# Kernel tuning notes

Measured on AMD Instinct MI355X. Metric: run time of the kernel, lower is better.

## Reference

```python
import jax, jax.numpy as jnp
import numpy as np

DIM = 128
HEADS = 4
WIN = (2, 7, 7)
N = WIN[0] * WIN[1] * WIN[2]  # 98
NW = 64
B_ = 2048  # batch(32) * nW(64)
SCALE = (DIM // HEADS) ** -0.5


def _relative_position_index():
    d, h, w = WIN
    coords = np.stack(np.meshgrid(np.arange(d), np.arange(h), np.arange(w), indexing='ij'))
    cf = coords.reshape(3, -1)
    rel = (cf[:, :, None] - cf[:, None, :]).transpose(1, 2, 0)
    rel[:, :, 0] += d - 1
    rel[:, :, 1] += h - 1
    rel[:, :, 2] += w - 1
    rel[:, :, 0] *= (2 * h - 1) * (2 * w - 1)
    rel[:, :, 1] *= 2 * w - 1
    return rel.sum(-1).astype(np.int32)  # [N, N]


def setup_inputs() -> dict:
    key = jax.random.key(0)
    ks = jax.random.split(key, 8)
    table_rows = (2 * WIN[0] - 1) * (2 * WIN[1] - 1) * (2 * WIN[2] - 1)  # 507
    return {
        "x": jax.random.normal(ks[0], (B_, N, DIM), jnp.float32),
        "mask": jax.random.normal(ks[1], (NW, N, N), jnp.float32),
        "qkv_w": jax.random.normal(ks[2], (DIM, 3 * DIM), jnp.float32) * 0.02,
        "qkv_b": jnp.zeros((3 * DIM,), jnp.float32),
        "rel_bias_table": jax.random.normal(ks[3], (table_rows, HEADS), jnp.float32) * 0.02,
        "rel_index": jnp.asarray(_relative_position_index()),
        "proj_w": jax.random.normal(ks[4], (DIM, DIM), jnp.float32) * 0.02,
        "proj_b": jnp.zeros((DIM,), jnp.float32),
    }


def reference(x, mask, qkv_w, qkv_b, rel_bias_table, rel_index, proj_w, proj_b):
    B, n, C = x.shape
    H = HEADS
    hd = C // H
    qkv = x @ qkv_w + qkv_b                              # [B, N, 3C]
    qkv = qkv.reshape(B, n, 3, H, hd).transpose(2, 0, 3, 1, 4)  # [3, B, H, N, hd]
    q, k, v = qkv[0] * SCALE, qkv[1], qkv[2]
    attn = jnp.einsum('bhnd,bhmd->bhnm', q, k)           # [B, H, N, N]
    bias = rel_bias_table[rel_index.reshape(-1)].reshape(n, n, H).transpose(2, 0, 1)
    attn = attn + bias[None]
    nW = mask.shape[0]
    attn = attn.reshape(B // nW, nW, H, n, n) + mask[None, :, None]
    attn = attn.reshape(B, H, n, n)
    attn = jax.nn.softmax(attn, axis=-1)
    out = jnp.einsum('bhnm,bhmd->bnhd', attn, v).reshape(B, n, C)
    return out @ proj_w + proj_b
```

## Files before the change

kernel.cpp:

```cpp
#include <hip/hip_runtime.h>
#include <hip/hip_bf16.h>

typedef __bf16 bf16;
typedef __attribute__((ext_vector_type(8))) __bf16 bf16x8;
typedef __attribute__((ext_vector_type(4))) __bf16 bf16x4;
typedef __attribute__((ext_vector_type(2))) __bf16 bf16x2;
typedef __attribute__((ext_vector_type(4))) float f32x4;

#define NTOK 98
#define NP   112
#define DIM  128
#define NH   4
#define HD   32
#define SCALE_Q 0.17677669529663687f

#define SXP 136
#define SKP 40
#define SVP 136
#define SPP 136
#define SQP 40
#define STGP 40
#define HREG 2560

#define WS_WTQ  0ULL
#define WS_PT   98304ULL
#define WS_BM   131072ULL
#define WS_NEED 12976128ULL

__global__ __launch_bounds__(256) void prep3_kernel(
    const float* __restrict__ qkv_w, const float* __restrict__ proj_w,
    const float* __restrict__ table, const int* __restrict__ rel,
    const float* __restrict__ mask,
    bf16* __restrict__ WTq, bf16* __restrict__ PT2, float* __restrict__ bmt)
{
  int i = blockIdx.x * 256 + threadIdx.x;
  if (i < 384*128) {
    int n = i >> 7, k = i & 127;
    WTq[i] = (bf16)qkv_w[k*384 + n];
  } else if (i < 384*128 + 128*128) {
    int j = i - 384*128; int n = j >> 7, kp = j & 127;
    int blk = kp >> 5, jl = kp & 31;
    int dl = (jl >> 1) + 16*(jl & 1);
    PT2[j] = (bf16)proj_w[(blk*32 + dl)*128 + n];
  } else {
    int g = i - (384*128 + 128*128);
    if (g >= 64*4*112*112) return;
    int k = g % 112;
    int rest = g / 112;
    int q = rest % 112;
    int rest2 = rest / 112;
    int h = rest2 & 3;
    int w = rest2 >> 2;
    float v;
    if (k >= NTOK) v = -1.0e30f;
    else if (q >= NTOK) v = 0.f;
    else v = table[rel[q*98 + k]*4 + h] + mask[w*9604 + q*98 + k];
    bmt[g] = v;
  }
}

__global__ __launch_bounds__(256, 3) void fused_kernel(
    const float* __restrict__ x, const float* __restrict__ qkv_b,
    const float* __restrict__ proj_b,
    const bf16* __restrict__ WTq, const bf16* __restrict__ PT2,
    const float* __restrict__ bmt, float* __restrict__ out)
{
  __shared__ alignas(16) bf16 sA[NP*SXP];
  __shared__ alignas(16) bf16 sB[4*HREG];

  const int b = blockIdx.x, w = b & 63;
  const int tid = threadIdx.x;
  const int wave = tid >> 6, lane = tid & 63;
  const int quad = lane >> 4, l16 = lane & 15;
  const int h = wave;
  const f32x4 fzero = {0.f, 0.f, 0.f, 0.f};

  {
    const float* xb = x + (size_t)b * (NTOK*DIM);
    for (int i = tid; i < NTOK*32; i += 256) {
      int row = i >> 5, c4 = (i & 31) << 2;
      const float4 v = *(const float4*)(xb + row*DIM + c4);
      bf16x4 pk; pk[0]=(bf16)v.x; pk[1]=(bf16)v.y; pk[2]=(bf16)v.z; pk[3]=(bf16)v.w;
      *(bf16x4*)&sA[row*SXP + c4] = pk;
    }
    for (int i = tid; i < 14*32; i += 256) {
      int row = NTOK + (i >> 5), c4 = (i & 31) << 2;
      uint2 z; z.x = 0; z.y = 0;
      *(uint2*)&sA[row*SXP + c4] = z;
    }
  }
  __syncthreads();

  bf16* stg = sB + h*HREG;
  bf16x8 bk[7], aq[7], bv[2][4];

  {
    const int baseK = DIM + h*HD, baseQ = h*HD;
    bf16x8 wK0[4], wK1[4], wQ0[4], wQ1[4];
#pragma unroll
    for (int ks = 0; ks < 4; ++ks) {
      wK0[ks] = *(const bf16x8*)(WTq + (baseK + l16)*DIM + ks*32 + quad*8);
      wK1[ks] = *(const bf16x8*)(WTq + (baseK + 16 + l16)*DIM + ks*32 + quad*8);
      wQ0[ks] = *(const bf16x8*)(WTq + (baseQ + l16)*DIM + ks*32 + quad*8);
      wQ1[ks] = *(const bf16x8*)(WTq + (baseQ + 16 + l16)*DIM + ks*32 + quad*8);
    }
    const float cK0 = qkv_b[baseK + l16], cK1 = qkv_b[baseK + 16 + l16];
    const float cQ0 = qkv_b[baseQ + l16], cQ1 = qkv_b[baseQ + 16 + l16];
#pragma unroll
    for (int mt = 0; mt < 7; ++mt) {
      f32x4 k0 = fzero, k1 = fzero, q0 = fzero, q1 = fzero;
#pragma unroll
      for (int ks = 0; ks < 4; ++ks) {
        const bf16x8 a = *(const bf16x8*)&sA[(mt*16 + l16)*SXP + ks*32 + quad*8];
        k0 = __builtin_amdgcn_mfma_f32_16x16x32_bf16(a, wK0[ks], k0, 0, 0, 0);
        k1 = __builtin_amdgcn_mfma_f32_16x16x32_bf16(a, wK1[ks], k1, 0, 0, 0);
        q0 = __builtin_amdgcn_mfma_f32_16x16x32_bf16(a, wQ0[ks], q0, 0, 0, 0);
        q1 = __builtin_amdgcn_mfma_f32_16x16x32_bf16(a, wQ1[ks], q1, 0, 0, 0);
      }
#pragma unroll
      for (int r = 0; r < 4; ++r) {
        bf16x2 pk; pk[0] = (bf16)(k0[r] + cK0); pk[1] = (bf16)(k1[r] + cK1);
        *(bf16x2*)&stg[(quad*4 + r)*STGP + l16*2] = pk;
        bf16x2 pq; pq[0] = (bf16)((q0[r] + cQ0) * SCALE_Q);
        pq[1] = (bf16)((q1[r] + cQ1) * SCALE_Q);
        *(bf16x2*)&stg[(16 + quad*4 + r)*STGP + l16*2] = pq;
      }
      bk[mt] = *(const bf16x8*)&stg[l16*STGP + quad*8];
      aq[mt] = *(const bf16x8*)&stg[(16 + l16)*STGP + quad*8];
    }
  }

  {
    const int baseV = 2*DIM + h*HD;
    bf16x8 wV0[4], wV1[4];
#pragma unroll
    for (int ks = 0; ks < 4; ++ks) {
      wV0[ks] = *(const bf16x8*)(WTq + (baseV + l16)*DIM + ks*32 + quad*8);
      wV1[ks] = *(const bf16x8*)(WTq + (baseV + 16 + l16)*DIM + ks*32 + quad*8);
    }
    const float cV0 = qkv_b[baseV + l16], cV1 = qkv_b[baseV + 16 + l16];
#pragma unroll
    for (int ck = 0; ck < 4; ++ck) {
      bf16* vb = stg + (ck & 1)*1280;
#pragma unroll
      for (int hf = 0; hf < 2; ++hf) {
        const int mt = ck*2 + hf;
        if (mt < 7) {
          f32x4 a0 = fzero, a1 = fzero;
#pragma unroll
          for (int ks = 0; ks < 4; ++ks) {
            const bf16x8 a = *(const bf16x8*)&sA[(mt*16 + l16)*SXP + ks*32 + quad*8];
            a0 = __builtin_amdgcn_mfma_f32_16x16x32_bf16(a, wV0[ks], a0, 0, 0, 0);
            a1 = __builtin_amdgcn_mfma_f32_16x16x32_bf16(a, wV1[ks], a1, 0, 0, 0);
          }
          bf16x4 p0, p1;
#pragma unroll
          for (int r = 0; r < 4; ++r) { p0[r] = (bf16)(a0[r] + cV0); p1[r] = (bf16)(a1[r] + cV1); }
          *(bf16x4*)&vb[l16*STGP + hf*16 + quad*4] = p0;
          *(bf16x4*)&vb[(16 + l16)*STGP + hf*16 + quad*4] = p1;
        } else {
          uint2 z; z.x = 0; z.y = 0;
          *(uint2*)&vb[l16*STGP + hf*16 + quad*4] = z;
          *(uint2*)&vb[(16 + l16)*STGP + hf*16 + quad*4] = z;
        }
      }
      bv[0][ck] = *(const bf16x8*)&vb[l16*STGP + quad*8];
      bv[1][ck] = *(const bf16x8*)&vb[(16 + l16)*STGP + quad*8];
    }
  }
  __syncthreads();

  bf16* sP = stg;
  {
    int row = lane >> 2, c0 = 112 + ((lane & 3) << 2);
    uint2 z; z.x = 0; z.y = 0;
    *(uint2*)&sP[row*SPP + c0] = z;
  }
  const float* bmh = bmt + ((size_t)(w*4 + h))*(NP*NP);

#pragma unroll
  for (int mt = 0; mt < 7; ++mt) {
    f32x4 s[7];
#pragma unroll
    for (int nt = 0; nt < 7; ++nt)
      s[nt] = __builtin_amdgcn_mfma_f32_16x16x32_bf16(bk[nt], aq[mt], fzero, 0, 0, 0);
    const float* bq = bmh + (mt*16 + l16)*NP;
#pragma unroll
    for (int nt = 0; nt < 7; ++nt) {
      const f32x4 bm4 = *(const f32x4*)(bq + nt*16 + quad*4);
      s[nt] = s[nt] + bm4;
    }
#pragma unroll
    for (int nt = 0; nt < 7; ++nt)
#pragma unroll
      for (int r = 0; r < 4; ++r)
        s[nt][r] = __expf(s[nt][r]);
#pragma unroll
    for (int nt = 0; nt < 7; ++nt) {
      bf16x4 pk;
#pragma unroll
      for (int r = 0; r < 4; ++r) pk[r] = (bf16)s[nt][r];
      *(bf16x4*)&sP[l16*SPP + nt*16 + quad*4] = pk;
    }
    float rs[7];
#pragma unroll
    for (int nt = 0; nt < 7; ++nt)
      rs[nt] = (s[nt][0] + s[nt][1]) + (s[nt][2] + s[nt][3]);
    float sum = ((rs[0] + rs[1]) + (rs[2] + rs[3])) + ((rs[4] + rs[5]) + rs[6]);
    sum += __shfl_xor(sum, 16);
    sum += __shfl_xor(sum, 32);
    const float inv = __builtin_amdgcn_rcpf(sum);
    float invr[4];
#pragma unroll
    for (int r = 0; r < 4; ++r)
      invr[r] = __shfl(inv, quad*4 + r, 64);
    f32x4 o0 = fzero, o1 = fzero;
#pragma unroll
    for (int ks = 0; ks < 4; ++ks) {
      const bf16x8 ap = *(const bf16x8*)&sP[l16*SPP + ks*32 + quad*8];
      o0 = __builtin_amdgcn_mfma_f32_16x16x32_bf16(ap, bv[0][ks], o0, 0, 0, 0);
      o1 = __builtin_amdgcn_mfma_f32_16x16x32_bf16(ap, bv[1][ks], o1, 0, 0, 0);
    }
#pragma unroll
    for (int r = 0; r < 4; ++r) {
      bf16x2 ow; ow[0] = (bf16)(o0[r]*invr[r]); ow[1] = (bf16)(o1[r]*invr[r]);
      *(bf16x2*)&sA[(mt*16 + quad*4 + r)*SXP + h*HD + l16*2] = ow;
    }
  }
  __syncthreads();

  float* outb = out + (size_t)b * (NTOK*DIM);
#pragma unroll
  for (int nn = 0; nn < 2; ++nn) {
    const int nt2 = wave + nn*4;
    bf16x8 pf[4];
#pragma unroll
    for (int ks = 0; ks < 4; ++ks)
      pf[ks] = *(const bf16x8*)(PT2 + (nt2*16 + l16)*DIM + ks*32 + quad*8);
    const float pb = proj_b[nt2*16 + l16];
#pragma unroll
    for (int mt = 0; mt < 7; ++mt) {
      f32x4 acc = fzero;
#pragma unroll
      for (int ks = 0; ks < 4; ++ks) {
        const bf16x8 a = *(const bf16x8*)&sA[(mt*16 + l16)*SXP + ks*32 + quad*8];
        acc = __builtin_amdgcn_mfma_f32_16x16x32_bf16(a, pf[ks], acc, 0, 0, 0);
      }
#pragma unroll
      for (int r = 0; r < 4; ++r) {
        const int row = mt*16 + quad*4 + r;
        if (row < NTOK)
          outb[row*DIM + nt2*16 + l16] = acc[r] + pb;
      }
    }
  }
}


__global__ __launch_bounds__(256) void prep_kernel(
    const float* __restrict__ qkv_w, const float* __restrict__ proj_w,
    const float* __restrict__ table, const int* __restrict__ rel_index,
    bf16* __restrict__ WTq, bf16* __restrict__ PT, float* __restrict__ biasf)
{
  int i = blockIdx.x * 256 + threadIdx.x;
  if (i < 384*128) {
    int n = i >> 7, k = i & 127;
    WTq[i] = (bf16)qkv_w[k*384 + n];
  } else if (i < 384*128 + 128*128) {
    int j = i - 384*128; int n = j >> 7, k = j & 127;
    PT[j] = (bf16)proj_w[k*128 + n];
  } else if (i < 384*128 + 128*128 + 98*98) {
    int j = i - (384*128 + 128*128);
    int idx = rel_index[j];
#pragma unroll
    for (int h = 0; h < 4; ++h) biasf[h*9604 + j] = table[idx*4 + h];
  }
}

__global__ __launch_bounds__(512, 2) void win_attn_kernel(
    const float* __restrict__ x, const float* __restrict__ mask,
    const float* __restrict__ qkv_b, const float* __restrict__ proj_b,
    const bf16* __restrict__ WTq, const bf16* __restrict__ PT,
    const float* __restrict__ biasf, float* __restrict__ out)
{
  __shared__ bf16 sX[NP*SXP];
  __shared__ bf16 sK[NH*NP*SKP];
  __shared__ bf16 sVT[NH*HD*SVP];
  __shared__ bf16 sQs[8*16*SQP];
  __shared__ bf16 sPs[8*16*SPP];

  const int b = blockIdx.x;
  const int w = b & 63;
  const int tid = threadIdx.x;
  const int wave = tid >> 6, lane = tid & 63;
  const int quad = lane >> 4, l16 = lane & 15;
  const f32x4 fzero = {0.f, 0.f, 0.f, 0.f};

  {
    const float* xb = x + (size_t)b * (NTOK*DIM);
    for (int i = tid; i < NTOK*32; i += 512) {
      int row = i >> 5, c4 = (i & 31) << 2;
      const float4 v = *(const float4*)(xb + row*DIM + c4);
      bf16x4 pk; pk[0]=(bf16)v.x; pk[1]=(bf16)v.y; pk[2]=(bf16)v.z; pk[3]=(bf16)v.w;
      *(bf16x4*)&sX[row*SXP + c4] = pk;
    }
    for (int i = tid; i < 14*32; i += 512) {
      int row = NTOK + (i >> 5), c4 = (i & 31) << 2;
      uint2 z; z.x = 0; z.y = 0;
      *(uint2*)&sX[row*SXP + c4] = z;
    }
    {
      int h = tid >> 7, rem = tid & 127, d = rem >> 2, c0 = 112 + ((rem & 3) << 2);
      uint2 z; z.x = 0; z.y = 0;
      *(uint2*)&sVT[(h*HD + d)*SVP + c0] = z;
    }
  }
  __syncthreads();

#pragma unroll
  for (int j = 0; j < 2; ++j) {
    const int job = wave*2 + j;
    const int h = job >> 2, part = job & 3;
    const bool isK = part < 2;
    const int ncol = (isK ? DIM + h*HD + part*16 : 2*DIM + h*HD + (part-2)*16) + l16;
    bf16x8 bfr[4];
#pragma unroll
    for (int ks = 0; ks < 4; ++ks)
      bfr[ks] = *(const bf16x8*)(WTq + ncol*DIM + ks*32 + quad*8);
    const float cb = qkv_b[ncol];
#pragma unroll
    for (int mt = 0; mt < 7; ++mt) {
      f32x4 acc = fzero;
#pragma unroll
      for (int ks = 0; ks < 4; ++ks) {
        const bf16x8 a = *(const bf16x8*)&sX[(mt*16 + l16)*SXP + ks*32 + quad*8];
        acc = __builtin_amdgcn_mfma_f32_16x16x32_bf16(a, bfr[ks], acc, 0, 0, 0);
      }
      const int tb = mt*16 + quad*4;
      if (isK) {
        const int d = part*16 + l16;
#pragma unroll
        for (int r = 0; r < 4; ++r)
          sK[(h*NP + tb + r)*SKP + d] = (bf16)(acc[r] + cb);
      } else {
        const int d = (part-2)*16 + l16;
        bf16x4 pk;
#pragma unroll
        for (int r = 0; r < 4; ++r) pk[r] = (bf16)(acc[r] + cb);
        *(bf16x4*)&sVT[(h*HD + d)*SVP + tb] = pk;
      }
    }
  }
  __syncthreads();

  {
    const int h = wave >> 1, sub = wave & 1;
    bf16x8 qb[2][4];
#pragma unroll
    for (int nt2 = 0; nt2 < 2; ++nt2)
#pragma unroll
      for (int ks = 0; ks < 4; ++ks)
        qb[nt2][ks] = *(const bf16x8*)(WTq + (h*HD + nt2*16 + l16)*DIM + ks*32 + quad*8);
    const float qbias0 = qkv_b[h*HD + l16];
    const float qbias1 = qkv_b[h*HD + 16 + l16];
    bf16* sQ = sQs + wave*16*SQP;
    bf16* sP = sPs + wave*16*SPP;
    {
      int row = lane >> 2, c0 = 112 + ((lane & 3) << 2);
      uint2 z; z.x = 0; z.y = 0;
      *(uint2*)&sP[row*SPP + c0] = z;
    }
    const float* bias_h = biasf + h*9604;
    const float* mask_w = mask + w*9604;

    f32x4 oacc0 = fzero, oacc1 = fzero;
#pragma unroll 1
    for (int it = 0; it < 4; ++it) {
      const int mt = sub + it*2;
      const bool valid = mt < 7;
      if (valid) {
        f32x4 qa0 = fzero, qa1 = fzero;
#pragma unroll
        for (int ks = 0; ks < 4; ++ks) {
          const bf16x8 a = *(const bf16x8*)&sX[(mt*16 + l16)*SXP + ks*32 + quad*8];
          qa0 = __builtin_amdgcn_mfma_f32_16x16x32_bf16(a, qb[0][ks], qa0, 0, 0, 0);
          qa1 = __builtin_amdgcn_mfma_f32_16x16x32_bf16(a, qb[1][ks], qa1, 0, 0, 0);
        }
#pragma unroll
        for (int r = 0; r < 4; ++r) {
          sQ[(quad*4 + r)*SQP + l16]      = (bf16)((qa0[r] + qbias0) * SCALE_Q);
          sQ[(quad*4 + r)*SQP + 16 + l16] = (bf16)((qa1[r] + qbias1) * SCALE_Q);
        }
        const bf16x8 aq = *(const bf16x8*)&sQ[l16*SQP + quad*8];
        f32x4 s[7];
#pragma unroll
        for (int nt = 0; nt < 7; ++nt) {
          const bf16x8 bk2 = *(const bf16x8*)&sK[(h*NP + nt*16 + l16)*SKP + quad*8];
          s[nt] = __builtin_amdgcn_mfma_f32_16x16x32_bf16(aq, bk2, fzero, 0, 0, 0);
        }
#pragma unroll
        for (int r = 0; r < 4; ++r) {
          const int row = mt*16 + quad*4 + r;
          const bool rowok = row < NTOK;
          float mx = -3.0e38f;
#pragma unroll
          for (int nt = 0; nt < 7; ++nt) {
            const int col = nt*16 + l16;
            float sv;
            if (rowok && col < NTOK)
              sv = s[nt][r] + bias_h[row*NTOK + col] + mask_w[row*NTOK + col];
            else
              sv = -1.0e30f;
            s[nt][r] = sv;
            mx = fmaxf(mx, sv);
          }
#pragma unroll
          for (int off = 1; off < 16; off <<= 1)
            mx = fmaxf(mx, __shfl_xor(mx, off, 64));
          float sum = 0.f;
#pragma unroll
          for (int nt = 0; nt < 7; ++nt) {
            const float p = __expf(s[nt][r] - mx);
            s[nt][r] = p;
            sum += p;
          }
#pragma unroll
          for (int off = 1; off < 16; off <<= 1)
            sum += __shfl_xor(sum, off, 64);
          const float inv = __builtin_amdgcn_rcpf(sum);
#pragma unroll
          for (int nt = 0; nt < 7; ++nt)
            sP[(quad*4 + r)*SPP + nt*16 + l16] = (bf16)(s[nt][r] * inv);
        }
        oacc0 = fzero; oacc1 = fzero;
#pragma unroll
        for (int ks = 0; ks < 4; ++ks) {
          const bf16x8 ap = *(const bf16x8*)&sP[l16*SPP + ks*32 + quad*8];
          const bf16x8 bv0 = *(const bf16x8*)&sVT[(h*HD + l16)*SVP + ks*32 + quad*8];
          const bf16x8 bv1 = *(const bf16x8*)&sVT[(h*HD + 16 + l16)*SVP + ks*32 + quad*8];
          oacc0 = __builtin_amdgcn_mfma_f32_16x16x32_bf16(ap, bv0, oacc0, 0, 0, 0);
          oacc1 = __builtin_amdgcn_mfma_f32_16x16x32_bf16(ap, bv1, oacc1, 0, 0, 0);
        }
      }
      __syncthreads();
      if (valid) {
#pragma unroll
        for (int r = 0; r < 4; ++r) {
          sX[(mt*16 + quad*4 + r)*SXP + h*HD + l16]      = (bf16)(oacc0[r]);
          sX[(mt*16 + quad*4 + r)*SXP + h*HD + 16 + l16] = (bf16)(oacc1[r]);
        }
      }
    }
  }
  __syncthreads();

  {
    const int nt = wave;
    bf16x8 pbf[4];
#pragma unroll
    for (int ks = 0; ks < 4; ++ks)
      pbf[ks] = *(const bf16x8*)(PT + (nt*16 + l16)*DIM + ks*32 + quad*8);
    const float pb = proj_b[nt*16 + l16];
    float* outb = out + (size_t)b * (NTOK*DIM);
#pragma unroll
    for (int mt = 0; mt < 7; ++mt) {
      f32x4 acc = fzero;
#pragma unroll
      for (int ks = 0; ks < 4; ++ks) {
        const bf16x8 a = *(const bf16x8*)&sX[(mt*16 + l16)*SXP + ks*32 + quad*8];
        acc = __builtin_amdgcn_mfma_f32_16x16x32_bf16(a, pbf[ks], acc, 0, 0, 0);
      }
#pragma unroll
      for (int r = 0; r < 4; ++r) {
        const int row = mt*16 + quad*4 + r;
        if (row < NTOK)
          outb[row*DIM + nt*16 + l16] = acc[r] + pb;
      }
    }
  }
}

extern "C" void kernel_launch(void* const* d_in, const int* in_sizes, int n_in,
                              void* d_out, int out_size, void* d_ws, size_t ws_size,
                              hipStream_t stream)
{
  const float* x      = (const float*)d_in[0];
  const float* mask   = (const float*)d_in[1];
  const float* qkv_w  = (const float*)d_in[2];
  const float* qkv_b  = (const float*)d_in[3];
  const float* table  = (const float*)d_in[4];
  const int*   rel    = (const int*)d_in[5];
  const float* proj_w = (const float*)d_in[6];
  const float* proj_b = (const float*)d_in[7];
  float* out = (float*)d_out;
  char* ws = (char*)d_ws;

  if (ws_size >= WS_NEED) {
    bf16*  WTq = (bf16*)(ws + WS_WTQ);
    bf16*  PT2 = (bf16*)(ws + WS_PT);
    float* bmt = (float*)(ws + WS_BM);

    const int prep_total = 384*128 + 128*128 + 64*4*112*112;
    prep3_kernel<<<(prep_total + 255)/256, 256, 0, stream>>>(
        qkv_w, proj_w, table, rel, mask, WTq, PT2, bmt);
    fused_kernel<<<2048, 256, 0, stream>>>(x, qkv_b, proj_b, WTq, PT2, bmt, out);
  } else {
    bf16*  WTq   = (bf16*)(ws + WS_WTQ);
    bf16*  PT    = (bf16*)(ws + WS_PT);
    float* biasf = (float*)(ws + WS_BM);
    const int prep_total = 384*128 + 128*128 + 98*98;
    prep_kernel<<<(prep_total + 255)/256, 256, 0, stream>>>(qkv_w, proj_w, table, rel, WTq, PT, biasf);
    win_attn_kernel<<<2048, 512, 0, stream>>>(x, mask, qkv_b, proj_b, WTq, PT, biasf, out);
  }
}
```

Baseline: 281.3 us.

## Prefetch bias rows, use exp2 with folded log2e, add MFMA priority hints

The precomputed bias/mask table is now scaled by log2(e), and the Q scale absorbs log2(e), so the softmax can use the native exp2 instruction instead of __expf. The prep kernel writes the bias table four floats per thread with vector stores. In the attention loop, the next row-tile's bias is prefetched into registers while the current tile is processed, and the PV MFMA is issued before the row-sum reduction. s_setprio brackets around MFMA blocks favour matrix issue across waves. The cost is more live registers, which could hurt occupancy at 3 blocks per SM.

```diff
diff --git a/kernel.cpp b/kernel.cpp
--- a/kernel.cpp
+++ b/kernel.cpp
@@ -12,6 +12,8 @@
 #define DIM  128
 #define NH   4
 #define HD   32
+#define LOG2E 1.4426950408889634f
+#define SCALE_Q2 (0.17677669529663687f * 1.4426950408889634f)
 #define SCALE_Q 0.17677669529663687f
 
 #define SXP 136
@@ -26,6 +28,9 @@
 #define WS_PT   98304ULL
 #define WS_BM   131072ULL
 #define WS_NEED 12976128ULL
+
+#define PREP_SCALAR (384*128 + 128*128)
+#define PREP_BM_V4  (64*4*112*28)
 
 __global__ __launch_bounds__(256) void prep3_kernel(
     const float* __restrict__ qkv_w, const float* __restrict__ proj_w,
@@ -37,25 +42,32 @@
   if (i < 384*128) {
     int n = i >> 7, k = i & 127;
     WTq[i] = (bf16)qkv_w[k*384 + n];
-  } else if (i < 384*128 + 128*128) {
+  } else if (i < PREP_SCALAR) {
     int j = i - 384*128; int n = j >> 7, kp = j & 127;
     int blk = kp >> 5, jl = kp & 31;
     int dl = (jl >> 1) + 16*(jl & 1);
     PT2[j] = (bf16)proj_w[(blk*32 + dl)*128 + n];
   } else {
-    int g = i - (384*128 + 128*128);
-    if (g >= 64*4*112*112) return;
-    int k = g % 112;
-    int rest = g / 112;
+    int g = i - PREP_SCALAR;
+    if (g >= PREP_BM_V4) return;
+    int k4 = (g % 28) * 4;
+    int rest = g / 28;
     int q = rest % 112;
     int rest2 = rest / 112;
     int h = rest2 & 3;
     int w = rest2 >> 2;
-    float v;
-    if (k >= NTOK) v = -1.0e30f;
-    else if (q >= NTOK) v = 0.f;
-    else v = table[rel[q*98 + k]*4 + h] + mask[w*9604 + q*98 + k];
-    bmt[g] = v;
+    f32x4 v;
+    if (q >= NTOK) {
+      v[0] = 0.f; v[1] = 0.f; v[2] = 0.f; v[3] = 0.f;
+    } else {
+#pragma unroll
+      for (int j = 0; j < 4; ++j) {
+        int k = k4 + j;
+        if (k >= NTOK) v[j] = -1.0e30f;
+        else v[j] = (table[rel[q*98 + k]*4 + h] + mask[w*9604 + q*98 + k]) * LOG2E;
+      }
+    }
+    *(f32x4*)(bmt + ((size_t)(w*4 + h))*(NP*NP) + q*NP + k4) = v;
   }
 }
 
@@ -109,6 +121,7 @@
 #pragma unroll
     for (int mt = 0; mt < 7; ++mt) {
       f32x4 k0 = fzero, k1 = fzero, q0 = fzero, q1 = fzero;
+      __builtin_amdgcn_s_setprio(1);
 #pragma unroll
       for (int ks = 0; ks < 4; ++ks) {
         const bf16x8 a = *(const bf16x8*)&sA[(mt*16 + l16)*SXP + ks*32 + quad*8];
@@ -117,12 +130,13 @@
         q0 = __builtin_amdgcn_mfma_f32_16x16x32_bf16(a, wQ0[ks], q0, 0, 0, 0);
         q1 = __builtin_amdgcn_mfma_f32_16x16x32_bf16(a, wQ1[ks], q1, 0, 0, 0);
       }
+      __builtin_amdgcn_s_setprio(0);
 #pragma unroll
       for (int r = 0; r < 4; ++r) {
         bf16x2 pk; pk[0] = (bf16)(k0[r] + cK0); pk[1] = (bf16)(k1[r] + cK1);
         *(bf16x2*)&stg[(quad*4 + r)*STGP + l16*2] = pk;
-        bf16x2 pq; pq[0] = (bf16)((q0[r] + cQ0) * SCALE_Q);
-        pq[1] = (bf16)((q1[r] + cQ1) * SCALE_Q);
+        bf16x2 pq; pq[0] = (bf16)((q0[r] + cQ0) * SCALE_Q2);
+        pq[1] = (bf16)((q1[r] + cQ1) * SCALE_Q2);
         *(bf16x2*)&stg[(16 + quad*4 + r)*STGP + l16*2] = pq;
       }
       bk[mt] = *(const bf16x8*)&stg[l16*STGP + quad*8];
@@ -147,12 +161,14 @@
         const int mt = ck*2 + hf;
         if (mt < 7) {
           f32x4 a0 = fzero, a1 = fzero;
+          __builtin_amdgcn_s_setprio(1);
 #pragma unroll
           for (int ks = 0; ks < 4; ++ks) {
             const bf16x8 a = *(const bf16x8*)&sA[(mt*16 + l16)*SXP + ks*32 + quad*8];
             a0 = __builtin_amdgcn_mfma_f32_16x16x32_bf16(a, wV0[ks], a0, 0, 0, 0);
             a1 = __builtin_amdgcn_mfma_f32_16x16x32_bf16(a, wV1[ks], a1, 0, 0, 0);
           }
+          __builtin_amdgcn_s_setprio(0);
           bf16x4 p0, p1;
 #pragma unroll
           for (int r = 0; r < 4; ++r) { p0[r] = (bf16)(a0[r] + cV0); p1[r] = (bf16)(a1[r] + cV1); }
@@ -178,23 +194,33 @@
   }
   const float* bmh = bmt + ((size_t)(w*4 + h))*(NP*NP);
 
+  f32x4 bmc[7];
+#pragma unroll
+  for (int nt = 0; nt < 7; ++nt)
+    bmc[nt] = *(const f32x4*)(bmh + l16*NP + nt*16 + quad*4);
+
 #pragma unroll
   for (int mt = 0; mt < 7; ++mt) {
     f32x4 s[7];
+    __builtin_amdgcn_s_setprio(1);
 #pragma unroll
     for (int nt = 0; nt < 7; ++nt)
       s[nt] = __builtin_amdgcn_mfma_f32_16x16x32_bf16(bk[nt], aq[mt], fzero, 0, 0, 0);
-    const float* bq = bmh + (mt*16 + l16)*NP;
+    __builtin_amdgcn_s_setprio(0);
+    f32x4 bmn[7];
+    if (mt < 6) {
+      const float* bqn = bmh + ((mt+1)*16 + l16)*NP;
+#pragma unroll
+      for (int nt = 0; nt < 7; ++nt)
+        bmn[nt] = *(const f32x4*)(bqn + nt*16 + quad*4);
+    }
 #pragma unroll
     for (int nt = 0; nt < 7; ++nt) {
-      const f32x4 bm4 = *(const f32x4*)(bq + nt*16 + quad*4);
-      s[nt] = s[nt] + bm4;
-    }
-#pragma unroll
-    for (int nt = 0; nt < 7; ++nt)
+      s[nt] = s[nt] + bmc[nt];
 #pragma unroll
       for (int r = 0; r < 4; ++r)
-        s[nt][r] = __expf(s[nt][r]);
+        s[nt][r] = __builtin_amdgcn_exp2f(s[nt][r]);
+    }
 #pragma unroll
     for (int nt = 0; nt < 7; ++nt) {
       bf16x4 pk;
@@ -202,6 +228,15 @@
       for (int r = 0; r < 4; ++r) pk[r] = (bf16)s[nt][r];
       *(bf16x4*)&sP[l16*SPP + nt*16 + quad*4] = pk;
     }
+    f32x4 o0 = fzero, o1 = fzero;
+    __builtin_amdgcn_s_setprio(1);
+#pragma unroll
+    for (int ks = 0; ks < 4; ++ks) {
+      const bf16x8 ap = *(const bf16x8*)&sP[l16*SPP + ks*32 + quad*8];
+      o0 = __builtin_amdgcn_mfma_f32_16x16x32_bf16(ap, bv[0][ks], o0, 0, 0, 0);
+      o1 = __builtin_amdgcn_mfma_f32_16x16x32_bf16(ap, bv[1][ks], o1, 0, 0, 0);
+    }
+    __builtin_amdgcn_s_setprio(0);
     float rs[7];
 #pragma unroll
     for (int nt = 0; nt < 7; ++nt)
@@ -214,18 +249,15 @@
 #pragma unroll
     for (int r = 0; r < 4; ++r)
       invr[r] = __shfl(inv, quad*4 + r, 64);
-    f32x4 o0 = fzero, o1 = fzero;
-#pragma unroll
-    for (int ks = 0; ks < 4; ++ks) {
-      const bf16x8 ap = *(const bf16x8*)&sP[l16*SPP + ks*32 + quad*8];
-      o0 = __builtin_amdgcn_mfma_f32_16x16x32_bf16(ap, bv[0][ks], o0, 0, 0, 0);
-      o1 = __builtin_amdgcn_mfma_f32_16x16x32_bf16(ap, bv[1][ks], o1, 0, 0, 0);
-    }
 #pragma unroll
     for (int r = 0; r < 4; ++r) {
       bf16x2 ow; ow[0] = (bf16)(o0[r]*invr[r]); ow[1] = (bf16)(o1[r]*invr[r]);
       *(bf16x2*)&sA[(mt*16 + quad*4 + r)*SXP + h*HD + l16*2] = ow;
     }
+    if (mt < 6) {
+#pragma unroll
+      for (int nt = 0; nt < 7; ++nt) bmc[nt] = bmn[nt];
+    }
   }
   __syncthreads();
 
@@ -241,11 +273,13 @@
 #pragma unroll
     for (int mt = 0; mt < 7; ++mt) {
       f32x4 acc = fzero;
+      __builtin_amdgcn_s_setprio(1);
 #pragma unroll
       for (int ks = 0; ks < 4; ++ks) {
         const bf16x8 a = *(const bf16x8*)&sA[(mt*16 + l16)*SXP + ks*32 + quad*8];
         acc = __builtin_amdgcn_mfma_f32_16x16x32_bf16(a, pf[ks], acc, 0, 0, 0);
       }
+      __builtin_amdgcn_s_setprio(0);
 #pragma unroll
       for (int r = 0; r < 4; ++r) {
         const int row = mt*16 + quad*4 + r;
@@ -500,7 +534,7 @@
     bf16*  PT2 = (bf16*)(ws + WS_PT);
     float* bmt = (float*)(ws + WS_BM);
 
-    const int prep_total = 384*128 + 128*128 + 64*4*112*112;
+    const int prep_total = PREP_SCALAR + PREP_BM_V4;
     prep3_kernel<<<(prep_total + 255)/256, 256, 0, stream>>>(
         qkv_w, proj_w, table, rel, mask, WTq, PT2, bmt);
     fused_kernel<<<2048, 256, 0, stream>>>(x, qkv_b, proj_b, WTq, PT2, bmt, out);
```

Measured after the change: 307.3 us. 9.3% more time.
